# Kernel tuning notes

Hardware: AMD Instinct MI355X
Metric: run time of the kernel (lower is better)

The kernel has to match this reference:

```python
import jax, jax.numpy as jnp
import numpy as np

N, C_IN, T, V = 64, 64, 256, 25
S = 3            # num_subsets
C_OUT = 128
GROUPS = 8
EPS = 1e-5


def setup_inputs() -> dict:
    key = jax.random.key(0)
    ks = jax.random.split(key, 6)
    x = jax.random.normal(ks[0], (N, C_IN, T, V), dtype=jnp.float32)
    A = jax.random.uniform(ks[1], (S, V, V), dtype=jnp.float32) / V  # normalized-ish adjacency buffer
    PA = jax.random.normal(ks[2], (S, V, V), dtype=jnp.float32) * 0.01  # learnable adjacency offset
    cin_g = C_IN // GROUPS  # 8 input channels per group
    Wg = jax.random.normal(ks[3], (C_OUT * S, cin_g), dtype=jnp.float32) * (1.0 / np.sqrt(cin_g))
    bg = jax.random.normal(ks[4], (C_OUT * S,), dtype=jnp.float32) * 0.01
    gamma = jnp.ones((C_OUT,), dtype=jnp.float32)
    beta = jnp.zeros((C_OUT,), dtype=jnp.float32)
    return {"x": x, "A": A, "PA": PA, "Wg": Wg, "bg": bg, "gamma": gamma, "beta": beta}


def reference(x, A, PA, Wg, bg, gamma, beta):
    n, c, t, v = x.shape
    cin_g = c // GROUPS
    cout_total = Wg.shape[0]          # C_OUT * S
    cout_g = cout_total // GROUPS
    # grouped 1x1 conv: conv_group
    xg = x.reshape(n, GROUPS, cin_g, t, v)
    Wg_ = Wg.reshape(GROUPS, cout_g, cin_g)
    out = jnp.einsum('ngctv,gdc->ngdtv', xg, Wg_).reshape(n, cout_total, t, v)
    out = out + bg[None, :, None, None]
    # split into subsets and apply per-subset adjacency, accumulate
    outs = out.reshape(n, S, cout_total // S, t, v)   # (N,S,Cout,T,V)
    Aeff = A + PA                                      # (S,V,V)
    total = jnp.einsum('nsctv,svw->nctw', outs, Aeff)  # (N,Cout,T,V)
    # BatchNorm2d (training-mode batch statistics, biased variance)
    mean = total.mean(axis=(0, 2, 3), keepdims=True)
    var = ((total - mean) ** 2).mean(axis=(0, 2, 3), keepdims=True)
    y = (total - mean) * jax.lax.rsqrt(var + EPS)
    return y * gamma[None, :, None, None] + beta[None, :, None, None]
```

## Files before the change

### kernel.cpp

```cpp
#include <hip/hip_runtime.h>
#include <math.h>

#define NB   64
#define CIN  64
#define TDIM 256
#define VV   25
#define SS   3
#define COUT 128
#define NTV  (NB * TDIM * VV)
#define OUT_TOTAL (NB * COUT * TDIM * VV)
#define TT   8
#define NTILE (TDIM / TT)

#define WS_STATS 0
#define WS_AE2   2048
#define WS_W2    4160
#define WS_BIAS  7232
#define WS_SCALE 10816
#define WS_SHIFT 10944
#define MID_OFF  16384

__device__ __forceinline__ void fma4(float4& a, float s, const float4& b) {
    a.x = fmaf(s, b.x, a.x);
    a.y = fmaf(s, b.y, a.y);
    a.z = fmaf(s, b.z, a.z);
    a.w = fmaf(s, b.w, a.w);
}

__global__ void prep_kernel(const float* __restrict__ A, const float* __restrict__ PA,
                            const float* __restrict__ Wg, const float* __restrict__ bg,
                            float* __restrict__ ws) {
    const int gid = blockIdx.x * 256 + threadIdx.x;
    const int gstride = gridDim.x * 256;
    for (int i = gid; i < 2048; i += gstride) ws[WS_STATS + i] = 0.0f;
    for (int i = gid; i < 25 * 84; i += gstride) {
        int v = i / 84, r = i % 84;
        int s = r / 28, w = r % 28;
        float val = 0.0f;
        if (w < 25) {
            int idx = s * 625 + v * 25 + w;
            val = A[idx] + PA[idx];
        }
        ws[WS_AE2 + i] = val;
    }
    for (int i = gid; i < 24 * 128; i += gstride) {
        int row = i / 128, c = i % 128;
        int s = row / 8, j = row % 8;
        ws[WS_W2 + i] = Wg[(s * 128 + c) * 8 + j];
    }
    for (int i = gid; i < 128 * 28; i += gstride) {
        int c = i / 28, w = i % 28;
        float val = 0.0f;
        if (w < 25) {
            for (int s = 0; s < 3; ++s) {
                float cs = 0.0f;
                for (int v = 0; v < 25; ++v) {
                    int idx = s * 625 + v * 25 + w;
                    cs += A[idx] + PA[idx];
                }
                val += bg[s * 128 + c] * cs;
            }
        }
        ws[WS_BIAS + i] = val;
    }
}

template <bool PERM>
__global__ __launch_bounds__(256, 2)
void main_kernel(const float* __restrict__ x, float* __restrict__ ws,
                 float* __restrict__ out, float* __restrict__ mid) {
    __shared__ __align__(16) float s_x[25 * 68];
    __shared__ __align__(16) float s_ae[25 * 84];
    __shared__ __align__(16) float s_w[24 * 128];
    __shared__ __align__(16) float s_y[3 * 64 * 28];
    __shared__ __align__(16) float s_res[128 * 25];
    __shared__ float s_stats[256];

    const int tid = threadIdx.x;
    const int bid = blockIdx.x;
    const int xcd   = bid & 7;
    const int j     = bid >> 3;
    const int ttile = xcd * 4 + (j & 3);
    const int n     = j >> 2;
    const int t0    = ttile * TT;

    s_stats[tid] = 0.0f;
    for (int i = tid; i < 25 * 84; i += 256) s_ae[i] = ws[WS_AE2 + i];
    for (int i = tid; i < 24 * 128; i += 256) s_w[i] = ws[WS_W2 + i];

    const bool active = tid < 224;
    int c0 = 0, w0 = 0;
    float4 b0 = {0,0,0,0}, b1 = b0, b2 = b0, b3 = b0;
    if (active) {
        int ct = tid & 31, wt = tid >> 5;
        c0 = ct * 4;
        w0 = wt * 4;
        b0 = *(const float4*)&ws[WS_BIAS + (c0 + 0) * 28 + w0];
        b1 = *(const float4*)&ws[WS_BIAS + (c0 + 1) * 28 + w0];
        b2 = *(const float4*)&ws[WS_BIAS + (c0 + 2) * 28 + w0];
        b3 = *(const float4*)&ws[WS_BIAS + (c0 + 3) * 28 + w0];
    }
    float st1[4] = {0, 0, 0, 0};
    float st2[4] = {0, 0, 0, 0};

    const float* xbase = x + (size_t)n * (CIN * TDIM * VV);
    float* obase = out + (size_t)n * (COUT * TDIM * VV);
    float* mbase = mid + ((size_t)n * NTILE + ttile) * (TT * COUT * VV);

    {
        const float* xb = xbase + (size_t)t0 * VV;
        for (int i = tid; i < 64 * 25; i += 256) {
            int cin = i / 25, v = i % 25;
            s_x[v * 68 + cin] = xb[cin * (TDIM * VV) + v];
        }
    }
    __syncthreads();

    for (int task = tid; task < 336; task += 256) {
        int cint = task & 15, swt = task >> 4;
        int cin0 = cint * 4, sw0 = swt * 4;
        float4 a0 = {0, 0, 0, 0}, a1 = a0, a2 = a0, a3 = a0;
        #pragma unroll
        for (int v = 0; v < 25; ++v) {
            float4 xv = *(const float4*)&s_x[v * 68 + cin0];
            float4 av = *(const float4*)&s_ae[v * 84 + sw0];
            fma4(a0, xv.x, av);
            fma4(a1, xv.y, av);
            fma4(a2, xv.z, av);
            fma4(a3, xv.w, av);
        }
        int s = sw0 / 28, w = sw0 % 28;
        int yb = (s * 64 + cin0) * 28 + w;
        *(float4*)&s_y[yb]      = a0;
        *(float4*)&s_y[yb + 28] = a1;
        *(float4*)&s_y[yb + 56] = a2;
        *(float4*)&s_y[yb + 84] = a3;
    }
    __syncthreads();

    for (int tt = 0; tt < TT; ++tt) {
        float xr[7];
        if (tt < TT - 1) {
            const float* xb = xbase + (size_t)(t0 + tt + 1) * VV;
            #pragma unroll
            for (int m = 0; m < 7; ++m) {
                int i = tid + 256 * m;
                if (i < 1600) {
                    int cin = i / 25, v = i - cin * 25;
                    xr[m] = xb[cin * (TDIM * VV) + v];
                }
            }
        }

        if (active) {
            float4 r0 = b0, r1 = b1, r2 = b2, r3 = b3;
            #pragma unroll
            for (int s = 0; s < 3; ++s) {
                int g = (s * 128 + c0) / 48;
                int yb = (s * 64 + g * 8) * 28 + w0;
                int wb = s * 8 * 128 + c0;
                #pragma unroll
                for (int jj = 0; jj < 8; ++jj) {
                    float4 wv = *(const float4*)&s_w[wb + jj * 128];
                    float4 yv = *(const float4*)&s_y[yb + jj * 28];
                    fma4(r0, wv.x, yv);
                    fma4(r1, wv.y, yv);
                    fma4(r2, wv.z, yv);
                    fma4(r3, wv.w, yv);
                }
            }
            float4 rr[4] = {r0, r1, r2, r3};
            #pragma unroll
            for (int a = 0; a < 4; ++a) {
                float4 v = rr[a];
                if (w0 + 3 < 25) {
                    st1[a] += v.x + v.y + v.z + v.w;
                    st2[a] += v.x * v.x + v.y * v.y + v.z * v.z + v.w * v.w;
                } else {
                    st1[a] += v.x;
                    st2[a] += v.x * v.x;
                }
            }
            #pragma unroll
            for (int a = 0; a < 4; ++a) {
                int base = (c0 + a) * 25 + w0;
                s_res[base] = rr[a].x;
                if (w0 + 3 < 25) {
                    s_res[base + 1] = rr[a].y;
                    s_res[base + 2] = rr[a].z;
                    s_res[base + 3] = rr[a].w;
                }
            }
        }

        if (tt < TT - 1) {
            #pragma unroll
            for (int m = 0; m < 7; ++m) {
                int i = tid + 256 * m;
                if (i < 1600) {
                    int cin = i / 25, v = i - cin * 25;
                    s_x[v * 68 + cin] = xr[m];
                }
            }
        }
        __syncthreads();

        if (PERM) {
            float4* mb = (float4*)(mbase + tt * (COUT * VV));
            const float4* sr = (const float4*)s_res;
            for (int i = tid; i < 128 * 25 / 4; i += 256) mb[i] = sr[i];
        } else {
            float* ob = obase + (size_t)(t0 + tt) * VV;
            for (int i = tid; i < 128 * 25; i += 256) {
                int c = i / 25, w = i % 25;
                ob[c * (TDIM * VV) + w] = s_res[i];
            }
        }

        if (tt < TT - 1) {
            for (int task = tid; task < 336; task += 256) {
                int cint = task & 15, swt = task >> 4;
                int cin0 = cint * 4, sw0 = swt * 4;
                float4 a0 = {0, 0, 0, 0}, a1 = a0, a2 = a0, a3 = a0;
                #pragma unroll
                for (int v = 0; v < 25; ++v) {
                    float4 xv = *(const float4*)&s_x[v * 68 + cin0];
                    float4 av = *(const float4*)&s_ae[v * 84 + sw0];
                    fma4(a0, xv.x, av);
                    fma4(a1, xv.y, av);
                    fma4(a2, xv.z, av);
                    fma4(a3, xv.w, av);
                }
                int s = sw0 / 28, w = sw0 % 28;
                int yb = (s * 64 + cin0) * 28 + w;
                *(float4*)&s_y[yb]      = a0;
                *(float4*)&s_y[yb + 28] = a1;
                *(float4*)&s_y[yb + 56] = a2;
                *(float4*)&s_y[yb + 84] = a3;
            }
        }
        __syncthreads();
    }

    if (active) {
        #pragma unroll
        for (int a = 0; a < 4; ++a) {
            atomicAdd(&s_stats[c0 + a], st1[a]);
            atomicAdd(&s_stats[128 + c0 + a], st2[a]);
        }
    }
    __syncthreads();
    if (tid < 128) {
        float* st = ws + WS_STATS + xcd * 256;
        atomicAdd(&st[tid], s_stats[tid]);
        atomicAdd(&st[128 + tid], s_stats[128 + tid]);
    }
}

__global__ void finalize_kernel(const float* __restrict__ gamma,
                                const float* __restrict__ beta,
                                float* __restrict__ ws) {
    const int c = threadIdx.x;
    if (c < 128) {
        float s = 0.0f, q = 0.0f;
        for (int k = 0; k < 8; ++k) {
            s += ws[WS_STATS + k * 256 + c];
            q += ws[WS_STATS + k * 256 + 128 + c];
        }
        const float inv = 1.0f / (float)NTV;
        float mean = s * inv;
        float var = q * inv - mean * mean;
        float sc = gamma[c] * rsqrtf(var + 1e-5f);
        ws[WS_SCALE + c] = sc;
        ws[WS_SHIFT + c] = beta[c] - mean * sc;
    }
}

__global__ __launch_bounds__(256)
void norm_perm(const float* __restrict__ mid, float* __restrict__ out,
               const float* __restrict__ ws) {
    __shared__ __align__(16) float sb[6400];
    const int tid = threadIdx.x;
    const int bid = blockIdx.x;
    const int n  = bid >> 5;
    const int cq = bid & 31;
    const int c0 = cq * 4;

    float sca[4], sha[4];
    #pragma unroll
    for (int cl = 0; cl < 4; ++cl) {
        sca[cl] = ws[WS_SCALE + c0 + cl];
        sha[cl] = ws[WS_SHIFT + c0 + cl];
    }

    const float* mb = mid + (size_t)n * (TDIM * COUT * VV) + c0 * VV;
    for (int tc = 0; tc < 4; ++tc) {
        const float* mc = mb + (size_t)tc * 64 * (COUT * VV);
        #pragma unroll
        for (int k = 0; k < 7; ++k) {
            int idx = k * 256 + tid;
            if (idx < 1600) {
                int t = idx / 25;
                int q = idx - t * 25;
                float4 v = *(const float4*)&mc[(size_t)t * (COUT * VV) + q * 4];
                *(float4*)&sb[idx * 4] = v;
            }
        }
        __syncthreads();
        #pragma unroll
        for (int cl = 0; cl < 4; ++cl) {
            float4* ob4 = (float4*)(out + ((size_t)(n * COUT + c0 + cl)) * (TDIM * VV)
                                        + tc * 1600);
            const float sc = sca[cl], sh = sha[cl];
            #pragma unroll
            for (int k = 0; k < 2; ++k) {
                int j4 = k * 256 + tid;
                if (j4 < 400) {
                    int jb = j4 * 4;
                    float4 r;
                    {
                        int t = (jb + 0) / 25, v = (jb + 0) - t * 25;
                        r.x = fmaf(sb[t * 100 + cl * 25 + v], sc, sh);
                    }
                    {
                        int t = (jb + 1) / 25, v = (jb + 1) - t * 25;
                        r.y = fmaf(sb[t * 100 + cl * 25 + v], sc, sh);
                    }
                    {
                        int t = (jb + 2) / 25, v = (jb + 2) - t * 25;
                        r.z = fmaf(sb[t * 100 + cl * 25 + v], sc, sh);
                    }
                    {
                        int t = (jb + 3) / 25, v = (jb + 3) - t * 25;
                        r.w = fmaf(sb[t * 100 + cl * 25 + v], sc, sh);
                    }
                    ob4[j4] = r;
                }
            }
        }
        __syncthreads();
    }
}

__global__ __launch_bounds__(256)
void norm_inplace(float* __restrict__ out, const float* __restrict__ ws) {
    const int total4 = OUT_TOTAL / 4;
    const int stride = gridDim.x * blockDim.x;
    for (int i = blockIdx.x * blockDim.x + threadIdx.x; i < total4; i += stride) {
        int c = (i / 1600) & 127;
        float sc = ws[WS_SCALE + c];
        float sh = ws[WS_SHIFT + c];
        float4 v = ((float4*)out)[i];
        v.x = fmaf(v.x, sc, sh);
        v.y = fmaf(v.y, sc, sh);
        v.z = fmaf(v.z, sc, sh);
        v.w = fmaf(v.w, sc, sh);
        ((float4*)out)[i] = v;
    }
}

extern "C" void kernel_launch(void* const* d_in, const int* in_sizes, int n_in,
                              void* d_out, int out_size, void* d_ws, size_t ws_size,
                              hipStream_t stream) {
    const float* x     = (const float*)d_in[0];
    const float* A     = (const float*)d_in[1];
    const float* PA    = (const float*)d_in[2];
    const float* Wg    = (const float*)d_in[3];
    const float* bg    = (const float*)d_in[4];
    const float* gamma = (const float*)d_in[5];
    const float* beta  = (const float*)d_in[6];
    float* out = (float*)d_out;
    float* ws  = (float*)d_ws;
    float* mid = ws + MID_OFF;

    const bool perm = ws_size >= ((size_t)MID_OFF + (size_t)OUT_TOTAL) * sizeof(float);

    prep_kernel<<<64, 256, 0, stream>>>(A, PA, Wg, bg, ws);
    if (perm) {
        main_kernel<true><<<NB * NTILE, 256, 0, stream>>>(x, ws, out, mid);
        finalize_kernel<<<1, 128, 0, stream>>>(gamma, beta, ws);
        norm_perm<<<NB * 32, 256, 0, stream>>>(mid, out, ws);
    } else {
        main_kernel<false><<<NB * NTILE, 256, 0, stream>>>(x, ws, out, mid);
        finalize_kernel<<<1, 128, 0, stream>>>(gamma, beta, ws);
        norm_inplace<<<4096, 256, 0, stream>>>(out, ws);
    }
}
```

Before: 1.071 ms.

## Fold BN finalize into norm_perm and split time chunks across more blocks

Removes the single-block finalize launch by having each norm_perm block reduce the per-channel partial statistics itself and compute its scale and shift. Also splits the four time chunks of the former per-block loop into separate blocks, raising the grid from 2048 to 8192 blocks and dropping the loop's barriers. The cost is redundant recomputation of the statistics reduction (16 small loads per channel) in every block.

```diff
diff --git a/kernel.cpp b/kernel.cpp
--- a/kernel.cpp
+++ b/kernel.cpp
@@ -278,67 +278,78 @@
 
 __global__ __launch_bounds__(256)
 void norm_perm(const float* __restrict__ mid, float* __restrict__ out,
-               const float* __restrict__ ws) {
+               const float* __restrict__ ws,
+               const float* __restrict__ gamma, const float* __restrict__ beta) {
     __shared__ __align__(16) float sb[6400];
     const int tid = threadIdx.x;
     const int bid = blockIdx.x;
-    const int n  = bid >> 5;
-    const int cq = bid & 31;
+    const int n  = bid >> 7;
+    const int r  = bid & 127;
+    const int cq = r >> 2;
+    const int tc = r & 3;
     const int c0 = cq * 4;
 
     float sca[4], sha[4];
     #pragma unroll
     for (int cl = 0; cl < 4; ++cl) {
-        sca[cl] = ws[WS_SCALE + c0 + cl];
-        sha[cl] = ws[WS_SHIFT + c0 + cl];
-    }
-
-    const float* mb = mid + (size_t)n * (TDIM * COUT * VV) + c0 * VV;
-    for (int tc = 0; tc < 4; ++tc) {
-        const float* mc = mb + (size_t)tc * 64 * (COUT * VV);
+        const int c = c0 + cl;
+        float s = 0.0f, q = 0.0f;
         #pragma unroll
-        for (int k = 0; k < 7; ++k) {
-            int idx = k * 256 + tid;
-            if (idx < 1600) {
-                int t = idx / 25;
-                int q = idx - t * 25;
-                float4 v = *(const float4*)&mc[(size_t)t * (COUT * VV) + q * 4];
-                *(float4*)&sb[idx * 4] = v;
-            }
-        }
-        __syncthreads();
+        for (int k = 0; k < 8; ++k) {
+            s += ws[WS_STATS + k * 256 + c];
+            q += ws[WS_STATS + k * 256 + 128 + c];
+        }
+        const float inv = 1.0f / (float)NTV;
+        float mean = s * inv;
+        float var = q * inv - mean * mean;
+        float sc = gamma[c] * rsqrtf(var + 1e-5f);
+        sca[cl] = sc;
+        sha[cl] = beta[c] - mean * sc;
+    }
+
+    const float* mc = mid + (size_t)n * (TDIM * COUT * VV) + c0 * VV
+                          + (size_t)tc * 64 * (COUT * VV);
+    #pragma unroll
+    for (int k = 0; k < 7; ++k) {
+        int idx = k * 256 + tid;
+        if (idx < 1600) {
+            int t = idx / 25;
+            int q = idx - t * 25;
+            float4 v = *(const float4*)&mc[(size_t)t * (COUT * VV) + q * 4];
+            *(float4*)&sb[idx * 4] = v;
+        }
+    }
+    __syncthreads();
+    #pragma unroll
+    for (int cl = 0; cl < 4; ++cl) {
+        float4* ob4 = (float4*)(out + ((size_t)(n * COUT + c0 + cl)) * (TDIM * VV)
+                                    + tc * 1600);
+        const float sc = sca[cl], sh = sha[cl];
         #pragma unroll
-        for (int cl = 0; cl < 4; ++cl) {
-            float4* ob4 = (float4*)(out + ((size_t)(n * COUT + c0 + cl)) * (TDIM * VV)
-                                        + tc * 1600);
-            const float sc = sca[cl], sh = sha[cl];
-            #pragma unroll
-            for (int k = 0; k < 2; ++k) {
-                int j4 = k * 256 + tid;
-                if (j4 < 400) {
-                    int jb = j4 * 4;
-                    float4 r;
-                    {
-                        int t = (jb + 0) / 25, v = (jb + 0) - t * 25;
-                        r.x = fmaf(sb[t * 100 + cl * 25 + v], sc, sh);
-                    }
-                    {
-                        int t = (jb + 1) / 25, v = (jb + 1) - t * 25;
-                        r.y = fmaf(sb[t * 100 + cl * 25 + v], sc, sh);
-                    }
-                    {
-                        int t = (jb + 2) / 25, v = (jb + 2) - t * 25;
-                        r.z = fmaf(sb[t * 100 + cl * 25 + v], sc, sh);
-                    }
-                    {
-                        int t = (jb + 3) / 25, v = (jb + 3) - t * 25;
-                        r.w = fmaf(sb[t * 100 + cl * 25 + v], sc, sh);
-                    }
-                    ob4[j4] = r;
-                }
-            }
-        }
-        __syncthreads();
+        for (int k = 0; k < 2; ++k) {
+            int j4 = k * 256 + tid;
+            if (j4 < 400) {
+                int jb = j4 * 4;
+                float4 rv;
+                {
+                    int t = (jb + 0) / 25, v = (jb + 0) - t * 25;
+                    rv.x = fmaf(sb[t * 100 + cl * 25 + v], sc, sh);
+                }
+                {
+                    int t = (jb + 1) / 25, v = (jb + 1) - t * 25;
+                    rv.y = fmaf(sb[t * 100 + cl * 25 + v], sc, sh);
+                }
+                {
+                    int t = (jb + 2) / 25, v = (jb + 2) - t * 25;
+                    rv.z = fmaf(sb[t * 100 + cl * 25 + v], sc, sh);
+                }
+                {
+                    int t = (jb + 3) / 25, v = (jb + 3) - t * 25;
+                    rv.w = fmaf(sb[t * 100 + cl * 25 + v], sc, sh);
+                }
+                ob4[j4] = rv;
+            }
+        }
     }
 }
 
@@ -378,8 +389,7 @@
     prep_kernel<<<64, 256, 0, stream>>>(A, PA, Wg, bg, ws);
     if (perm) {
         main_kernel<true><<<NB * NTILE, 256, 0, stream>>>(x, ws, out, mid);
-        finalize_kernel<<<1, 128, 0, stream>>>(gamma, beta, ws);
-        norm_perm<<<NB * 32, 256, 0, stream>>>(mid, out, ws);
+        norm_perm<<<NB * 128, 256, 0, stream>>>(mid, out, ws, gamma, beta);
     } else {
         main_kernel<false><<<NB * NTILE, 256, 0, stream>>>(x, ws, out, mid);
         finalize_kernel<<<1, 128, 0, stream>>>(gamma, beta, ws);
```

New measurement: 1.067 ms. Within noise of the previous version (-0.3%).
